# Kernel tuning notes

Hardware: AMD Instinct MI355X
Metric: run time of the kernel (lower is better)

Reference implementation:

```python
import jax, jax.numpy as jnp
import numpy as np

TEMPERATURE = 0.5
COS_EPS = 1e-8  # torch.nn.CosineSimilarity default eps


def setup_inputs() -> dict:
    key = jax.random.key(0)
    k1, k2 = jax.random.split(key)
    N, D = 4096, 128
    z_i = jax.random.normal(k1, (N, D), dtype=jnp.float32)
    z_j = jax.random.normal(k2, (N, D), dtype=jnp.float32)
    return {"z_i": z_i, "z_j": z_j}


def reference(z_i, z_j):
    t = TEMPERATURE
    # L2-normalize each row (torch.norm over dim=1, then divide)
    zi = z_i / jnp.linalg.norm(z_i, axis=1, keepdims=True)
    zj = z_j / jnp.linalg.norm(z_j, axis=1, keepdims=True)
    z_ij = jnp.concatenate([zi, zj], axis=0)  # [2N, D]
    z_ji = jnp.concatenate([zj, zi], axis=0)  # [2N, D]
    # Full pairwise similarity matrix, scaled by temperature: [2N, 2N]
    sim = jnp.matmul(z_ij, z_ij.T) / t
    exp_sim = jnp.exp(sim)
    exp_sum = jnp.sum(exp_sim, axis=1)          # row reduction
    diag = jnp.diagonal(exp_sim)                # self-similarity terms
    # numerator: exp(cosine_similarity(z_ij, z_ji) / t) — positive pairs
    cos = jnp.sum(z_ij * z_ji, axis=1) / jnp.maximum(
        jnp.linalg.norm(z_ij, axis=1) * jnp.linalg.norm(z_ji, axis=1), COS_EPS)
    numerator = jnp.exp(cos / t)
    denominator = exp_sum - diag
    loss = -jnp.log(numerator / denominator)
    return jnp.mean(loss)
```

## Files before the change

kernel.cpp:

```cpp
#include <hip/hip_runtime.h>
#include <hip/hip_bf16.h>

typedef __attribute__((ext_vector_type(8))) short short8;
typedef __attribute__((ext_vector_type(4))) float floatx4;

#define D_DIM 128
#define SCALE_F 1.6986436f
#define CS 16
#define CTILE 64
#define BLK_ROWS 256
#define MREP 4

typedef __attribute__((address_space(1))) const unsigned int GUI;
typedef __attribute__((address_space(3))) unsigned int LUI;
#define GLOAD16(g, l) __builtin_amdgcn_global_load_lds((GUI*)(g), (LUI*)(l), 16, 0, 0)

__global__ void prep_kernel(const float* __restrict__ zi,
                            const float* __restrict__ zj,
                            __hip_bfloat16* __restrict__ Zb,
                            float* __restrict__ posdot,
                            float* __restrict__ selfarg, int N) {
    int r = blockIdx.x * 4 + (threadIdx.x >> 6);
    int t = threadIdx.x & 63;
    const float* pi = zi + (size_t)r * D_DIM;
    const float* pj = zj + (size_t)r * D_DIM;
    float a0 = pi[t], a1 = pi[t + 64];
    float b0 = pj[t], b1 = pj[t + 64];
    float ssi = a0*a0 + a1*a1;
    float ssj = b0*b0 + b1*b1;
    float sij = a0*b0 + a1*b1;
#pragma unroll
    for (int off = 1; off < 64; off <<= 1) {
        ssi += __shfl_xor(ssi, off);
        ssj += __shfl_xor(ssj, off);
        sij += __shfl_xor(sij, off);
    }
    float ni = sqrtf(ssi), nj = sqrtf(ssj);
    float ri = SCALE_F / ni, rj = SCALE_F / nj;
    __hip_bfloat16 vi0 = __float2bfloat16(a0 * ri);
    __hip_bfloat16 vi1 = __float2bfloat16(a1 * ri);
    __hip_bfloat16 vj0 = __float2bfloat16(b0 * rj);
    __hip_bfloat16 vj1 = __float2bfloat16(b1 * rj);
    __hip_bfloat16* zr0 = Zb + (size_t)r * D_DIM;
    __hip_bfloat16* zr1 = Zb + (size_t)(r + N) * D_DIM;
    zr0[t]      = vi0;  zr0[t + 64] = vi1;
    zr1[t]      = vj0;  zr1[t + 64] = vj1;
    float fi0 = __bfloat162float(vi0), fi1 = __bfloat162float(vi1);
    float fj0 = __bfloat162float(vj0), fj1 = __bfloat162float(vj1);
    float sdi = fi0*fi0 + fi1*fi1;
    float sdj = fj0*fj0 + fj1*fj1;
#pragma unroll
    for (int off = 1; off < 64; off <<= 1) {
        sdi += __shfl_xor(sdi, off);
        sdj += __shfl_xor(sdj, off);
    }
    if (t == 0) {
        posdot[r] = sij / fmaxf(ni * nj, 1e-8f);
        selfarg[r]     = sdi;
        selfarg[r + N] = sdj;
    }
}

__global__ __launch_bounds__(512, 4)
void main_kernel(const ushort* __restrict__ Zu,
                 float* __restrict__ rowpart, int N2) {
    __shared__ ushort Btile[2][CTILE * D_DIM];

    const int tid  = threadIdx.x;
    const int lane = tid & 63;
    const int wave = tid >> 6;
    const int mw   = wave & 3;
    const int nh   = wave >> 2;
    const int m    = lane & 15;
    const int kg   = lane >> 4;
    const int rwave0 = blockIdx.x * BLK_ROWS + mw * 64;
    const int cy   = blockIdx.y;

    short8 afrag[MREP][4];
#pragma unroll
    for (int rb = 0; rb < MREP; ++rb) {
        const ushort* ap = Zu + (size_t)(rwave0 + rb * 16 + m) * D_DIM + kg * 8;
#pragma unroll
        for (int ks = 0; ks < 4; ++ks)
            afrag[rb][ks] = *(const short8*)(ap + ks * 32);
    }

    float rowacc[MREP][4];
#pragma unroll
    for (int rb = 0; rb < MREP; ++rb)
#pragma unroll
        for (int g = 0; g < 4; ++g) rowacc[rb][g] = 0.0f;

    const int cols_per_chunk = N2 / CS;
    const int ntile = cols_per_chunk / CTILE;
    const int c0base = cy * cols_per_chunk;

    const int row0 = tid >> 4,          slot0 = (tid & 15) ^ (row0 & 7);
    const int row1 = 32 + (tid >> 4),   slot1 = (tid & 15) ^ (row1 & 7);
    const ushort* gsrc0 = Zu + (size_t)(c0base + row0) * D_DIM + slot0 * 8;
    const ushort* gsrc1 = Zu + (size_t)(c0base + row1) * D_DIM + slot1 * 8;
    const size_t tadv = (size_t)CTILE * D_DIM;

    GLOAD16(gsrc0, &Btile[0][(size_t)tid * 8]);
    GLOAD16(gsrc1, &Btile[0][(size_t)(512 + tid) * 8]);
    __syncthreads();

    for (int t = 0; t < ntile; ++t) {
        if (t + 1 < ntile) {
            const ushort* g0 = gsrc0 + (size_t)(t + 1) * tadv;
            const ushort* g1 = gsrc1 + (size_t)(t + 1) * tadv;
            ushort* nbuf = Btile[(t + 1) & 1];
            GLOAD16(g0, &nbuf[(size_t)tid * 8]);
            GLOAD16(g1, &nbuf[(size_t)(512 + tid) * 8]);
        }

#pragma unroll
        for (int rb = 0; rb < MREP; ++rb)
#pragma unroll
            for (int ks = 0; ks < 4; ++ks)
                asm volatile("" : "+v"(afrag[rb][ks]));

        const ushort* buf = Btile[t & 1];
#pragma unroll
        for (int s2 = 0; s2 < 2; ++s2) {
            const int brow = nh * 32 + s2 * 16 + m;
            short8 bfrag[4];
#pragma unroll
            for (int ks = 0; ks < 4; ++ks) {
                int ss = (ks * 4 + kg) ^ (brow & 7);
                bfrag[ks] = *(const short8*)&buf[brow * D_DIM + ss * 8];
            }
#pragma unroll
            for (int rb = 0; rb < MREP; ++rb) {
                floatx4 ac0 = {0.f, 0.f, 0.f, 0.f};
                floatx4 ac1 = {0.f, 0.f, 0.f, 0.f};
                ac0 = __builtin_amdgcn_mfma_f32_16x16x32_bf16(afrag[rb][0], bfrag[0], ac0, 0, 0, 0);
                ac1 = __builtin_amdgcn_mfma_f32_16x16x32_bf16(afrag[rb][2], bfrag[2], ac1, 0, 0, 0);
                ac0 = __builtin_amdgcn_mfma_f32_16x16x32_bf16(afrag[rb][1], bfrag[1], ac0, 0, 0, 0);
                ac1 = __builtin_amdgcn_mfma_f32_16x16x32_bf16(afrag[rb][3], bfrag[3], ac1, 0, 0, 0);
#pragma unroll
                for (int g = 0; g < 4; ++g)
                    rowacc[rb][g] += __builtin_amdgcn_exp2f(ac0[g] + ac1[g]);
            }
        }
        __syncthreads();
    }

#pragma unroll
    for (int rb = 0; rb < MREP; ++rb)
#pragma unroll
        for (int g = 0; g < 4; ++g) {
            float v = rowacc[rb][g];
            v += __shfl_xor(v, 1);
            v += __shfl_xor(v, 2);
            v += __shfl_xor(v, 4);
            v += __shfl_xor(v, 8);
            if (m == 0) {
                int grow = rwave0 + rb * 16 + kg * 4 + g;
                rowpart[(size_t)(cy * 2 + nh) * N2 + grow] = v;
            }
        }
}

__global__ void finalize1_kernel(const float* __restrict__ rowpart,
                                 const float* __restrict__ selfarg,
                                 const float* __restrict__ posdot,
                                 float* __restrict__ bpart, int N2, int NP) {
    __shared__ float red[4];
    int tid = threadIdx.x;
    int r = blockIdx.x * 256 + tid;
    float denom = 0.0f;
#pragma unroll
    for (int q = 0; q < 2 * CS; ++q) denom += rowpart[(size_t)q * N2 + r];
    denom -= __builtin_amdgcn_exp2f(selfarg[r]);
    float pos = posdot[r < NP ? r : r - NP];
    float v = logf(denom) - 2.0f * pos;
#pragma unroll
    for (int off = 1; off < 64; off <<= 1) v += __shfl_xor(v, off);
    if ((tid & 63) == 0) red[tid >> 6] = v;
    __syncthreads();
    if (tid == 0) bpart[blockIdx.x] = red[0] + red[1] + red[2] + red[3];
}

__global__ void finalize2_kernel(const float* __restrict__ bpart,
                                 float* __restrict__ out, int nb, int N2) {
    int t = threadIdx.x;
    float v = (t < nb) ? bpart[t] : 0.0f;
#pragma unroll
    for (int off = 1; off < 64; off <<= 1) v += __shfl_xor(v, off);
    if (t == 0) out[0] = v / (float)N2;
}

extern "C" void kernel_launch(void* const* d_in, const int* in_sizes, int n_in,
                              void* d_out, int out_size, void* d_ws, size_t ws_size,
                              hipStream_t stream) {
    const float* zi = (const float*)d_in[0];
    const float* zj = (const float*)d_in[1];
    const int N  = in_sizes[0] / D_DIM;
    const int N2 = 2 * N;

    char* w = (char*)d_ws;
    __hip_bfloat16* Zb = (__hip_bfloat16*)w;
    size_t off = (size_t)N2 * D_DIM * sizeof(__hip_bfloat16);
    float* posdot  = (float*)(w + off);  off += (size_t)N  * sizeof(float);
    float* selfarg = (float*)(w + off);  off += (size_t)N2 * sizeof(float);
    float* rowpart = (float*)(w + off);  off += (size_t)(2 * CS) * N2 * sizeof(float);
    float* bpart   = (float*)(w + off);

    prep_kernel<<<N / 4, 256, 0, stream>>>(zi, zj, Zb, posdot, selfarg, N);
    dim3 grid(N2 / BLK_ROWS, CS);
    main_kernel<<<grid, 512, 0, stream>>>((const ushort*)Zb, rowpart, N2);
    const int nb = N2 / 256;
    finalize1_kernel<<<nb, 256, 0, stream>>>(rowpart, selfarg, posdot, bpart, N2, N);
    finalize2_kernel<<<1, 64, 0, stream>>>(bpart, (float*)d_out, nb, N2);
}
```

Before: 39.80 us.

## Exploit similarity symmetry: compute upper triangle with row and column partial sums

The main kernel now computes only the upper-triangular half of the 2N×2N exp-similarity matrix. Each block pairs a short and a long row-block strip to balance work, and it accumulates both row sums and column sums, with column partials written to a new workspace. The diagonal and lower part inside diagonal tiles are masked, which removes the self-term subtraction and the selfarg buffer. This roughly halves MFMA and exp work, but adds column shuffles and global writes, a larger colpart buffer and a longer finalize reduction.

```diff
diff --git a/kernel.cpp b/kernel.cpp
--- a/kernel.cpp
+++ b/kernel.cpp
@@ -8,8 +8,8 @@
 #define SCALE_F 1.6986436f
 #define CS 16
 #define CTILE 64
-#define BLK_ROWS 256
-#define MREP 4
+#define MREP 2
+#define NRXB 64
 
 typedef __attribute__((address_space(1))) const unsigned int GUI;
 typedef __attribute__((address_space(3))) unsigned int LUI;
@@ -18,8 +18,7 @@
 __global__ void prep_kernel(const float* __restrict__ zi,
                             const float* __restrict__ zj,
                             __hip_bfloat16* __restrict__ Zb,
-                            float* __restrict__ posdot,
-                            float* __restrict__ selfarg, int N) {
+                            float* __restrict__ posdot, int N) {
     int r = blockIdx.x * 4 + (threadIdx.x >> 6);
     int t = threadIdx.x & 63;
     const float* pi = zi + (size_t)r * D_DIM;
@@ -37,33 +36,19 @@
     }
     float ni = sqrtf(ssi), nj = sqrtf(ssj);
     float ri = SCALE_F / ni, rj = SCALE_F / nj;
-    __hip_bfloat16 vi0 = __float2bfloat16(a0 * ri);
-    __hip_bfloat16 vi1 = __float2bfloat16(a1 * ri);
-    __hip_bfloat16 vj0 = __float2bfloat16(b0 * rj);
-    __hip_bfloat16 vj1 = __float2bfloat16(b1 * rj);
     __hip_bfloat16* zr0 = Zb + (size_t)r * D_DIM;
     __hip_bfloat16* zr1 = Zb + (size_t)(r + N) * D_DIM;
-    zr0[t]      = vi0;  zr0[t + 64] = vi1;
-    zr1[t]      = vj0;  zr1[t + 64] = vj1;
-    float fi0 = __bfloat162float(vi0), fi1 = __bfloat162float(vi1);
-    float fj0 = __bfloat162float(vj0), fj1 = __bfloat162float(vj1);
-    float sdi = fi0*fi0 + fi1*fi1;
-    float sdj = fj0*fj0 + fj1*fj1;
-#pragma unroll
-    for (int off = 1; off < 64; off <<= 1) {
-        sdi += __shfl_xor(sdi, off);
-        sdj += __shfl_xor(sdj, off);
-    }
-    if (t == 0) {
-        posdot[r] = sij / fmaxf(ni * nj, 1e-8f);
-        selfarg[r]     = sdi;
-        selfarg[r + N] = sdj;
-    }
+    zr0[t]      = __float2bfloat16(a0 * ri);
+    zr0[t + 64] = __float2bfloat16(a1 * ri);
+    zr1[t]      = __float2bfloat16(b0 * rj);
+    zr1[t + 64] = __float2bfloat16(b1 * rj);
+    if (t == 0) posdot[r] = sij / fmaxf(ni * nj, 1e-8f);
 }
 
 __global__ __launch_bounds__(512, 4)
 void main_kernel(const ushort* __restrict__ Zu,
-                 float* __restrict__ rowpart, int N2) {
+                 float* __restrict__ rowpart,
+                 float* __restrict__ colpart, int N2) {
     __shared__ ushort Btile[2][CTILE * D_DIM];
 
     const int tid  = threadIdx.x;
@@ -73,97 +58,123 @@
     const int nh   = wave >> 2;
     const int m    = lane & 15;
     const int kg   = lane >> 4;
-    const int rwave0 = blockIdx.x * BLK_ROWS + mw * 64;
-    const int cy   = blockIdx.y;
-
-    short8 afrag[MREP][4];
-#pragma unroll
-    for (int rb = 0; rb < MREP; ++rb) {
-        const ushort* ap = Zu + (size_t)(rwave0 + rb * 16 + m) * D_DIM + kg * 8;
-#pragma unroll
-        for (int ks = 0; ks < 4; ++ks)
-            afrag[rb][ks] = *(const short8*)(ap + ks * 32);
-    }
-
-    float rowacc[MREP][4];
-#pragma unroll
-    for (int rb = 0; rb < MREP; ++rb)
-#pragma unroll
-        for (int g = 0; g < 4; ++g) rowacc[rb][g] = 0.0f;
-
-    const int cols_per_chunk = N2 / CS;
-    const int ntile = cols_per_chunk / CTILE;
-    const int c0base = cy * cols_per_chunk;
-
-    const int row0 = tid >> 4,          slot0 = (tid & 15) ^ (row0 & 7);
-    const int row1 = 32 + (tid >> 4),   slot1 = (tid & 15) ^ (row1 & 7);
-    const ushort* gsrc0 = Zu + (size_t)(c0base + row0) * D_DIM + slot0 * 8;
-    const ushort* gsrc1 = Zu + (size_t)(c0base + row1) * D_DIM + slot1 * 8;
-    const size_t tadv = (size_t)CTILE * D_DIM;
-
-    GLOAD16(gsrc0, &Btile[0][(size_t)tid * 8]);
-    GLOAD16(gsrc1, &Btile[0][(size_t)(512 + tid) * 8]);
-    __syncthreads();
-
-    for (int t = 0; t < ntile; ++t) {
-        if (t + 1 < ntile) {
-            const ushort* g0 = gsrc0 + (size_t)(t + 1) * tadv;
-            const ushort* g1 = gsrc1 + (size_t)(t + 1) * tadv;
-            ushort* nbuf = Btile[(t + 1) & 1];
-            GLOAD16(g0, &nbuf[(size_t)tid * 8]);
-            GLOAD16(g1, &nbuf[(size_t)(512 + tid) * 8]);
+    const int q    = blockIdx.y;
+    const int pair = blockIdx.x;
+    const int rxA  = pair;
+    const int rxB  = 63 - pair;
+    const int K1   = 128 - 2 * rxA;
+
+    const int srow0 = tid >> 4,        sslot0 = (tid & 15) ^ (srow0 & 7);
+    const int srow1 = 32 + (tid >> 4), sslot1 = (tid & 15) ^ (srow1 & 7);
+    const size_t tadv = (size_t)CS * CTILE * D_DIM;
+
+    for (int ph = 0; ph < 2; ++ph) {
+        const int rx0 = ph ? rxB : rxA;
+        const int K   = ph ? (128 - 2 * rxB) : K1;
+        const int k0  = ph ? ((q - K1) & 15) : q;
+        const int nt  = (K > k0) ? ((K - k0 + 15) >> 4) : 0;
+        const int rwave0 = rx0 * 128 + mw * 32;
+
+        short8 afrag[MREP][4];
+#pragma unroll
+        for (int rb = 0; rb < MREP; ++rb) {
+            const ushort* ap = Zu + (size_t)(rwave0 + rb * 16 + m) * D_DIM + kg * 8;
+#pragma unroll
+            for (int ks = 0; ks < 4; ++ks)
+                afrag[rb][ks] = *(const short8*)(ap + ks * 32);
         }
-
 #pragma unroll
         for (int rb = 0; rb < MREP; ++rb)
 #pragma unroll
             for (int ks = 0; ks < 4; ++ks)
                 asm volatile("" : "+v"(afrag[rb][ks]));
 
-        const ushort* buf = Btile[t & 1];
-#pragma unroll
-        for (int s2 = 0; s2 < 2; ++s2) {
-            const int brow = nh * 32 + s2 * 16 + m;
-            short8 bfrag[4];
-#pragma unroll
-            for (int ks = 0; ks < 4; ++ks) {
-                int ss = (ks * 4 + kg) ^ (brow & 7);
-                bfrag[ks] = *(const short8*)&buf[brow * D_DIM + ss * 8];
-            }
-#pragma unroll
-            for (int rb = 0; rb < MREP; ++rb) {
-                floatx4 ac0 = {0.f, 0.f, 0.f, 0.f};
-                floatx4 ac1 = {0.f, 0.f, 0.f, 0.f};
-                ac0 = __builtin_amdgcn_mfma_f32_16x16x32_bf16(afrag[rb][0], bfrag[0], ac0, 0, 0, 0);
-                ac1 = __builtin_amdgcn_mfma_f32_16x16x32_bf16(afrag[rb][2], bfrag[2], ac1, 0, 0, 0);
-                ac0 = __builtin_amdgcn_mfma_f32_16x16x32_bf16(afrag[rb][1], bfrag[1], ac0, 0, 0, 0);
-                ac1 = __builtin_amdgcn_mfma_f32_16x16x32_bf16(afrag[rb][3], bfrag[3], ac1, 0, 0, 0);
-#pragma unroll
-                for (int g = 0; g < 4; ++g)
-                    rowacc[rb][g] += __builtin_amdgcn_exp2f(ac0[g] + ac1[g]);
+        float rowacc[MREP][4];
+#pragma unroll
+        for (int rb = 0; rb < MREP; ++rb)
+#pragma unroll
+            for (int g = 0; g < 4; ++g) rowacc[rb][g] = 0.0f;
+
+        if (nt > 0) {
+            const int c0base = rx0 * 128 + k0 * 64;
+            const ushort* gsrc0 = Zu + (size_t)(c0base + srow0) * D_DIM + sslot0 * 8;
+            const ushort* gsrc1 = Zu + (size_t)(c0base + srow1) * D_DIM + sslot1 * 8;
+
+            GLOAD16(gsrc0, &Btile[0][(size_t)tid * 8]);
+            GLOAD16(gsrc1, &Btile[0][(size_t)(512 + tid) * 8]);
+            __syncthreads();
+
+            for (int t = 0; t < nt; ++t) {
+                if (t + 1 < nt) {
+                    ushort* nbuf = Btile[(t + 1) & 1];
+                    GLOAD16(gsrc0 + (size_t)(t + 1) * tadv, &nbuf[(size_t)tid * 8]);
+                    GLOAD16(gsrc1 + (size_t)(t + 1) * tadv, &nbuf[(size_t)(512 + tid) * 8]);
+                }
+
+                const ushort* buf = Btile[t & 1];
+                const int c0 = c0base + t * (CS * CTILE);
+                const bool dt = (t == 0) && (k0 < 2);
+
+#pragma unroll
+                for (int s2 = 0; s2 < 2; ++s2) {
+                    const int brow = nh * 32 + s2 * 16 + m;
+                    short8 bfrag[4];
+#pragma unroll
+                    for (int ks = 0; ks < 4; ++ks) {
+                        int ss = (ks * 4 + kg) ^ (brow & 7);
+                        bfrag[ks] = *(const short8*)&buf[brow * D_DIM + ss * 8];
+                    }
+                    const int gc = c0 + brow;
+                    float cf = 0.0f;
+#pragma unroll
+                    for (int rb = 0; rb < MREP; ++rb) {
+                        floatx4 ac0 = {0.f, 0.f, 0.f, 0.f};
+                        floatx4 ac1 = {0.f, 0.f, 0.f, 0.f};
+                        ac0 = __builtin_amdgcn_mfma_f32_16x16x32_bf16(afrag[rb][0], bfrag[0], ac0, 0, 0, 0);
+                        ac1 = __builtin_amdgcn_mfma_f32_16x16x32_bf16(afrag[rb][2], bfrag[2], ac1, 0, 0, 0);
+                        ac0 = __builtin_amdgcn_mfma_f32_16x16x32_bf16(afrag[rb][1], bfrag[1], ac0, 0, 0, 0);
+                        ac1 = __builtin_amdgcn_mfma_f32_16x16x32_bf16(afrag[rb][3], bfrag[3], ac1, 0, 0, 0);
+#pragma unroll
+                        for (int g = 0; g < 4; ++g) {
+                            float arg = ac0[g] + ac1[g];
+                            if (dt) {
+                                int gr = rwave0 + rb * 16 + kg * 4 + g;
+                                arg = (gc > gr) ? arg : -1000.0f;
+                            }
+                            float e = __builtin_amdgcn_exp2f(arg);
+                            rowacc[rb][g] += e;
+                            cf += e;
+                        }
+                    }
+                    cf += __shfl_xor(cf, 16);
+                    cf += __shfl_xor(cf, 32);
+                    if (lane < 16)
+                        colpart[(size_t)(rx0 * 4 + mw) * N2 + gc] = cf;
+                }
+                __syncthreads();
             }
         }
-        __syncthreads();
+
+#pragma unroll
+        for (int rb = 0; rb < MREP; ++rb)
+#pragma unroll
+            for (int g = 0; g < 4; ++g) {
+                float v = rowacc[rb][g];
+                v += __shfl_xor(v, 1);
+                v += __shfl_xor(v, 2);
+                v += __shfl_xor(v, 4);
+                v += __shfl_xor(v, 8);
+                if (m == 0) {
+                    int grow = rwave0 + rb * 16 + kg * 4 + g;
+                    rowpart[(size_t)(q * 2 + nh) * N2 + grow] = v;
+                }
+            }
+        if (ph == 0) __syncthreads();
     }
-
-#pragma unroll
-    for (int rb = 0; rb < MREP; ++rb)
-#pragma unroll
-        for (int g = 0; g < 4; ++g) {
-            float v = rowacc[rb][g];
-            v += __shfl_xor(v, 1);
-            v += __shfl_xor(v, 2);
-            v += __shfl_xor(v, 4);
-            v += __shfl_xor(v, 8);
-            if (m == 0) {
-                int grow = rwave0 + rb * 16 + kg * 4 + g;
-                rowpart[(size_t)(cy * 2 + nh) * N2 + grow] = v;
-            }
-        }
 }
 
 __global__ void finalize1_kernel(const float* __restrict__ rowpart,
-                                 const float* __restrict__ selfarg,
+                                 const float* __restrict__ colpart,
                                  const float* __restrict__ posdot,
                                  float* __restrict__ bpart, int N2, int NP) {
     __shared__ float red[4];
@@ -171,8 +182,10 @@
     int r = blockIdx.x * 256 + tid;
     float denom = 0.0f;
 #pragma unroll
-    for (int q = 0; q < 2 * CS; ++q) denom += rowpart[(size_t)q * N2 + r];
-    denom -= __builtin_amdgcn_exp2f(selfarg[r]);
+    for (int p = 0; p < 2 * CS; ++p) denom += rowpart[(size_t)p * N2 + r];
+    int nplanes = ((r >> 7) + 1) * 4;
+    for (int pl = 0; pl < nplanes; ++pl)
+        denom += colpart[(size_t)pl * N2 + r];
     float pos = posdot[r < NP ? r : r - NP];
     float v = logf(denom) - 2.0f * pos;
 #pragma unroll
@@ -203,14 +216,14 @@
     __hip_bfloat16* Zb = (__hip_bfloat16*)w;
     size_t off = (size_t)N2 * D_DIM * sizeof(__hip_bfloat16);
     float* posdot  = (float*)(w + off);  off += (size_t)N  * sizeof(float);
-    float* selfarg = (float*)(w + off);  off += (size_t)N2 * sizeof(float);
     float* rowpart = (float*)(w + off);  off += (size_t)(2 * CS) * N2 * sizeof(float);
+    float* colpart = (float*)(w + off);  off += (size_t)(NRXB * 4) * N2 * sizeof(float);
     float* bpart   = (float*)(w + off);
 
-    prep_kernel<<<N / 4, 256, 0, stream>>>(zi, zj, Zb, posdot, selfarg, N);
-    dim3 grid(N2 / BLK_ROWS, CS);
-    main_kernel<<<grid, 512, 0, stream>>>((const ushort*)Zb, rowpart, N2);
+    prep_kernel<<<N / 4, 256, 0, stream>>>(zi, zj, Zb, posdot, N);
+    dim3 grid(32, CS);
+    main_kernel<<<grid, 512, 0, stream>>>((const ushort*)Zb, rowpart, colpart, N2);
     const int nb = N2 / 256;
-    finalize1_kernel<<<nb, 256, 0, stream>>>(rowpart, selfarg, posdot, bpart, N2, N);
+    finalize1_kernel<<<nb, 256, 0, stream>>>(rowpart, colpart, posdot, bpart, N2, N);
     finalize2_kernel<<<1, 64, 0, stream>>>(bpart, (float*)d_out, nb, N2);
 }
```

New measurement: 90.50 us. +127.4%, slower.
